# Kernel tuning notes

Measured on AMD Instinct MI355X. Metric: run time of the kernel, lower is better.

Reference implementation:

```python
import jax, jax.numpy as jnp
import numpy as np

HID = 256
BN_EPS = 1e-5
LN_EPS = 1e-5


def setup_inputs() -> dict:
    key = jax.random.key(0)
    ks = jax.random.split(key, 32)
    N, E, B = 50000, 400000, 2048
    F_ATOM, F_PROT = 70, 480

    def lin(k, fi, fo):
        return jax.random.normal(k, (fi, fo), jnp.float32) / np.sqrt(fi).astype(np.float32)

    inp = {
        "x": jax.random.normal(ks[0], (N, F_ATOM), jnp.float32),
        "edge_index": jax.random.randint(ks[1], (2, E), 0, N, jnp.int64),
        "batch": jnp.sort(jax.random.randint(ks[2], (N,), 0, B, jnp.int64)),
        "protein_emb": jax.random.normal(ks[3], (B, F_PROT), jnp.float32),
        # GIN layer 0 (70 -> 256)
        "gin0_w1": lin(ks[4], F_ATOM, HID), "gin0_b1": jnp.zeros((HID,), jnp.float32),
        "gin0_w2": lin(ks[5], HID, HID),    "gin0_b2": jnp.zeros((HID,), jnp.float32),
        "gin0_gamma": jnp.ones((HID,), jnp.float32), "gin0_beta": jnp.zeros((HID,), jnp.float32),
        # GIN layers 1..3 stacked (256 -> 256)
        "gin_w1": jnp.stack([lin(ks[6 + i], HID, HID) for i in range(3)]),
        "gin_b1": jnp.zeros((3, HID), jnp.float32),
        "gin_w2": jnp.stack([lin(ks[9 + i], HID, HID) for i in range(3)]),
        "gin_b2": jnp.zeros((3, HID), jnp.float32),
        "gin_gamma": jnp.ones((3, HID), jnp.float32),
        "gin_beta": jnp.zeros((3, HID), jnp.float32),
        # protein projector
        "wp": lin(ks[12], F_PROT, HID), "bp": jnp.zeros((HID,), jnp.float32),
        "ln_g": jnp.ones((HID,), jnp.float32), "ln_b": jnp.zeros((HID,), jnp.float32),
        # predictor MLP
        "wpr1": lin(ks[13], 2 * HID, 1024), "bpr1": jnp.zeros((1024,), jnp.float32),
        "wpr2": lin(ks[14], 1024, 512),     "bpr2": jnp.zeros((512,), jnp.float32),
        "wpr3": lin(ks[15], 512, 1),        "bpr3": jnp.zeros((1,), jnp.float32),
    }
    return inp


def _gin_layer(h, src, dst, n_nodes, w1, b1, w2, b2, gamma, beta):
    # GINConv (eps=0): mlp(x + sum_{j->i} x_j); scatter-add over destination
    agg = jax.ops.segment_sum(h[src], dst, num_segments=n_nodes)
    z = h + agg
    z = jax.nn.relu(z @ w1 + b1) @ w2 + b2
    # BatchNorm1d in eval mode: running_mean=0, running_var=1
    z = z * (gamma / np.sqrt(1.0 + BN_EPS).astype(np.float32)) + beta
    return jax.nn.relu(z)  # dropout is identity in eval


def reference(x, edge_index, batch, protein_emb,
              gin0_w1, gin0_b1, gin0_w2, gin0_b2, gin0_gamma, gin0_beta,
              gin_w1, gin_b1, gin_w2, gin_b2, gin_gamma, gin_beta,
              wp, bp, ln_g, ln_b,
              wpr1, bpr1, wpr2, bpr2, wpr3, bpr3):
    n_nodes = x.shape[0]
    n_graphs = protein_emb.shape[0]
    src, dst = edge_index[0], edge_index[1]

    h = _gin_layer(x, src, dst, n_nodes, gin0_w1, gin0_b1, gin0_w2, gin0_b2, gin0_gamma, gin0_beta)
    for i in range(3):  # layers 1..3 with residual
        h = h + _gin_layer(h, src, dst, n_nodes,
                           gin_w1[i], gin_b1[i], gin_w2[i], gin_b2[i], gin_gamma[i], gin_beta[i])

    # global_add_pool over graph ids
    drug_vec = jax.ops.segment_sum(h, batch, num_segments=n_graphs)  # [B, 256]

    # protein projector: Linear -> LayerNorm -> ReLU (dropout identity)
    p = protein_emb @ wp + bp
    mu = jnp.mean(p, axis=-1, keepdims=True)
    var = jnp.var(p, axis=-1, keepdims=True)
    p = (p - mu) * jax.lax.rsqrt(var + LN_EPS) * ln_g + ln_b
    prot_vec = jax.nn.relu(p)

    cat = jnp.concatenate([drug_vec, prot_vec], axis=1)  # [B, 512]
    h1 = jax.nn.relu(cat @ wpr1 + bpr1)
    h2 = jax.nn.relu(h1 @ wpr2 + bpr2)
    return h2 @ wpr3 + bpr3  # [B, 1]
```

## Files before the change

### kernel.cpp

```cpp
#include <hip/hip_runtime.h>

#define F_ATOM 70

#define FLAG_RELU 1
#define FLAG_BN   2
#define FLAG_RES  4

typedef __attribute__((ext_vector_type(8))) short short8;
typedef __attribute__((ext_vector_type(4))) float floatx4;

__device__ __forceinline__ float bf2f(unsigned short u) {
    union { unsigned int i; float f; } x; x.i = (unsigned int)u << 16; return x.f;
}
__device__ __forceinline__ unsigned short f2bf(float f) {
    union { float f; unsigned int i; } x; x.f = f;
    unsigned int r = x.i + 0x7fffu + ((x.i >> 16) & 1u);
    return (unsigned short)(r >> 16);
}
__device__ __forceinline__ float blo(unsigned int u){ union{unsigned int a; float f;}x; x.a=u<<16; return x.f; }
__device__ __forceinline__ float bhi(unsigned int u){ union{unsigned int a; float f;}x; x.a=u&0xffff0000u; return x.f; }


__global__ void count_kernel(const int* __restrict__ dst, int* __restrict__ cnt, int E) {
    int i = blockIdx.x * blockDim.x + threadIdx.x;
    if (i < E) atomicAdd(&cnt[dst[i]], 1);
}

__global__ void scan_kernel(const int* __restrict__ cnt, int* __restrict__ offs, int n) {
    __shared__ int wsum[16];
    __shared__ int carry_s;
    int t = threadIdx.x, lane = t & 63, wid = t >> 6;
    if (t == 0) carry_s = 0;
    __syncthreads();
    for (int base = 0; base < n; base += 1024) {
        int idx = base + t;
        int v = (idx < n) ? cnt[idx] : 0;
        int s = v;
        #pragma unroll
        for (int o = 1; o < 64; o <<= 1) {
            int x = __shfl_up(s, o);
            if (lane >= o) s += x;
        }
        if (lane == 63) wsum[wid] = s;
        __syncthreads();
        int woff = 0;
        #pragma unroll
        for (int wI = 0; wI < 16; ++wI) woff += (wI < wid) ? wsum[wI] : 0;
        int carry = carry_s;
        if (idx < n) offs[idx] = carry + woff + s - v;
        __syncthreads();
        if (t == 1023) carry_s = carry + woff + s;
        __syncthreads();
    }
    if (threadIdx.x == 0) offs[n] = carry_s;
}

__global__ void fill_kernel(const int* __restrict__ src, const int* __restrict__ dst,
                            const int* __restrict__ offs, int* __restrict__ cursor,
                            int* __restrict__ ssrc, int E) {
    int i = blockIdx.x * blockDim.x + threadIdx.x;
    if (i < E) {
        int d = dst[i];
        int pos = atomicAdd(&cursor[d], 1);
        ssrc[offs[d] + pos] = src[i];
    }
}

__global__ void graph_bounds_kernel(const int* __restrict__ batch, int* __restrict__ goffs,
                                    int N, int B) {
    int g = blockIdx.x * blockDim.x + threadIdx.x;
    if (g > B) return;
    int lo = 0, hi = N;
    while (lo < hi) {
        int mid = (lo + hi) >> 1;
        if (batch[mid] < g) lo = mid + 1; else hi = mid;
    }
    goffs[g] = lo;
}


__global__ __launch_bounds__(256) void prep_kernel(
    const float* __restrict__ x, const float* __restrict__ pemb,
    const float* __restrict__ g0w1, const float* __restrict__ g0w2,
    const float* __restrict__ gw1, const float* __restrict__ gw2,
    const float* __restrict__ wp, const float* __restrict__ wpr1, const float* __restrict__ wpr2,
    unsigned short* __restrict__ xb, unsigned short* __restrict__ pembbf,
    unsigned short* __restrict__ w10t, unsigned short* __restrict__ w20t,
    unsigned short* __restrict__ w1t, unsigned short* __restrict__ w2t,
    unsigned short* __restrict__ wpt, unsigned short* __restrict__ wpr1t,
    unsigned short* __restrict__ wpr2t, int N, int B)
{
    const long long sz0 = (long long)N * 80;
    const long long sz1 = (long long)B * 480;
    const long long szw10 = 256 * 128, szw20 = 256 * 256;
    const long long szw1 = 3 * 256 * 256, szw2 = 3 * 256 * 256;
    const long long szwp = 256 * 480, szp1 = 1024 * 512, szp2 = 512 * 1024;
    const long long total = sz0 + sz1 + szw10 + szw20 + szw1 + szw2 + szwp + szp1 + szp2;
    const long long stride = (long long)gridDim.x * blockDim.x;
    for (long long idx = (long long)blockIdx.x * blockDim.x + threadIdx.x; idx < total; idx += stride) {
        long long r = idx;
        if (r < sz0) {
            int node = (int)(r / 80), f = (int)(r - (long long)node * 80);
            xb[r] = f2bf(f < F_ATOM ? x[(long long)node * F_ATOM + f] : 0.f);
            continue;
        }
        r -= sz0;
        if (r < sz1) { pembbf[r] = f2bf(pemb[r]); continue; }
        r -= sz1;
        if (r < szw10) {
            int nr = (int)(r >> 7), k = (int)(r & 127);
            w10t[r] = f2bf(k < F_ATOM ? g0w1[k * 256 + nr] : 0.f);
            continue;
        }
        r -= szw10;
        if (r < szw20) {
            int nr = (int)(r >> 8), k = (int)(r & 255);
            w20t[r] = f2bf(g0w2[k * 256 + nr]);
            continue;
        }
        r -= szw20;
        if (r < szw1) {
            int l = (int)(r >> 16); int r2 = (int)(r & 65535);
            int nr = r2 >> 8, k = r2 & 255;
            w1t[r] = f2bf(gw1[(size_t)l * 65536 + k * 256 + nr]);
            continue;
        }
        r -= szw1;
        if (r < szw2) {
            int l = (int)(r >> 16); int r2 = (int)(r & 65535);
            int nr = r2 >> 8, k = r2 & 255;
            w2t[r] = f2bf(gw2[(size_t)l * 65536 + k * 256 + nr]);
            continue;
        }
        r -= szw2;
        if (r < szwp) {
            int nr = (int)(r / 480), k = (int)(r - (long long)nr * 480);
            wpt[r] = f2bf(wp[k * 256 + nr]);
            continue;
        }
        r -= szwp;
        if (r < szp1) {
            int nr = (int)(r >> 9), k = (int)(r & 511);
            wpr1t[r] = f2bf(wpr1[k * 1024 + nr]);
            continue;
        }
        r -= szp1;
        {
            int nr = (int)(r >> 10), k = (int)(r & 1023);
            wpr2t[r] = f2bf(wpr2[k * 512 + nr]);
        }
    }
}

__global__ __launch_bounds__(256) void agg0b_kernel(
    const unsigned short* __restrict__ xb, const int* __restrict__ offs,
    const int* __restrict__ ssrc, unsigned short* __restrict__ z0, int n) {
    int t = threadIdx.x;
    int node = blockIdx.x * 16 + (t >> 4);
    if (node >= n) return;
    int c = t & 15;
    if (c >= 10) {
        *(uint4*)(z0 + (size_t)node * 128 + c * 8) = make_uint4(0, 0, 0, 0);
        return;
    }
    const unsigned short* base = xb + (size_t)node * 80 + c * 8;
    uint4 v = *(const uint4*)base;
    float a[8];
    a[0]=blo(v.x); a[1]=bhi(v.x); a[2]=blo(v.y); a[3]=bhi(v.y);
    a[4]=blo(v.z); a[5]=bhi(v.z); a[6]=blo(v.w); a[7]=bhi(v.w);
    int s = offs[node], e2 = offs[node + 1];
    int k = s;
    for (; k + 3 < e2; k += 4) {
        uint4 u0 = *(const uint4*)(xb + (size_t)ssrc[k]     * 80 + c * 8);
        uint4 u1 = *(const uint4*)(xb + (size_t)ssrc[k + 1] * 80 + c * 8);
        uint4 u2 = *(const uint4*)(xb + (size_t)ssrc[k + 2] * 80 + c * 8);
        uint4 u3 = *(const uint4*)(xb + (size_t)ssrc[k + 3] * 80 + c * 8);
        a[0]+=blo(u0.x); a[1]+=bhi(u0.x); a[2]+=blo(u0.y); a[3]+=bhi(u0.y);
        a[4]+=blo(u0.z); a[5]+=bhi(u0.z); a[6]+=blo(u0.w); a[7]+=bhi(u0.w);
        a[0]+=blo(u1.x); a[1]+=bhi(u1.x); a[2]+=blo(u1.y); a[3]+=bhi(u1.y);
        a[4]+=blo(u1.z); a[5]+=bhi(u1.z); a[6]+=blo(u1.w); a[7]+=bhi(u1.w);
        a[0]+=blo(u2.x); a[1]+=bhi(u2.x); a[2]+=blo(u2.y); a[3]+=bhi(u2.y);
        a[4]+=blo(u2.z); a[5]+=bhi(u2.z); a[6]+=blo(u2.w); a[7]+=bhi(u2.w);
        a[0]+=blo(u3.x); a[1]+=bhi(u3.x); a[2]+=blo(u3.y); a[3]+=bhi(u3.y);
        a[4]+=blo(u3.z); a[5]+=bhi(u3.z); a[6]+=blo(u3.w); a[7]+=bhi(u3.w);
    }
    for (; k < e2; ++k) {
        uint4 u0 = *(const uint4*)(xb + (size_t)ssrc[k] * 80 + c * 8);
        a[0]+=blo(u0.x); a[1]+=bhi(u0.x); a[2]+=blo(u0.y); a[3]+=bhi(u0.y);
        a[4]+=blo(u0.z); a[5]+=bhi(u0.z); a[6]+=blo(u0.w); a[7]+=bhi(u0.w);
    }
    unsigned int o0 = (unsigned int)f2bf(a[0]) | ((unsigned int)f2bf(a[1]) << 16);
    unsigned int o1 = (unsigned int)f2bf(a[2]) | ((unsigned int)f2bf(a[3]) << 16);
    unsigned int o2 = (unsigned int)f2bf(a[4]) | ((unsigned int)f2bf(a[5]) << 16);
    unsigned int o3 = (unsigned int)f2bf(a[6]) | ((unsigned int)f2bf(a[7]) << 16);
    *(uint4*)(z0 + (size_t)node * 128 + c * 8) = make_uint4(o0, o1, o2, o3);
}

__global__ __launch_bounds__(256) void agg_bf16_kernel(
    const unsigned short* __restrict__ h, const int* __restrict__ offs,
    const int* __restrict__ ssrc, unsigned short* __restrict__ out, int n) {
    int t = threadIdx.x;
    int node = blockIdx.x * 8 + (t >> 5);
    if (node >= n) return;
    int f8 = (t & 31) * 8;
    uint4 v = *(const uint4*)(h + (size_t)node * 256 + f8);
    float a[8];
    a[0]=blo(v.x); a[1]=bhi(v.x); a[2]=blo(v.y); a[3]=bhi(v.y);
    a[4]=blo(v.z); a[5]=bhi(v.z); a[6]=blo(v.w); a[7]=bhi(v.w);
    int s = offs[node], e2 = offs[node + 1];
    int k = s;
    for (; k + 3 < e2; k += 4) {
        uint4 u0 = *(const uint4*)(h + (size_t)ssrc[k]     * 256 + f8);
        uint4 u1 = *(const uint4*)(h + (size_t)ssrc[k + 1] * 256 + f8);
        uint4 u2 = *(const uint4*)(h + (size_t)ssrc[k + 2] * 256 + f8);
        uint4 u3 = *(const uint4*)(h + (size_t)ssrc[k + 3] * 256 + f8);
        a[0]+=blo(u0.x); a[1]+=bhi(u0.x); a[2]+=blo(u0.y); a[3]+=bhi(u0.y);
        a[4]+=blo(u0.z); a[5]+=bhi(u0.z); a[6]+=blo(u0.w); a[7]+=bhi(u0.w);
        a[0]+=blo(u1.x); a[1]+=bhi(u1.x); a[2]+=blo(u1.y); a[3]+=bhi(u1.y);
        a[4]+=blo(u1.z); a[5]+=bhi(u1.z); a[6]+=blo(u1.w); a[7]+=bhi(u1.w);
        a[0]+=blo(u2.x); a[1]+=bhi(u2.x); a[2]+=blo(u2.y); a[3]+=bhi(u2.y);
        a[4]+=blo(u2.z); a[5]+=bhi(u2.z); a[6]+=blo(u2.w); a[7]+=bhi(u2.w);
        a[0]+=blo(u3.x); a[1]+=bhi(u3.x); a[2]+=blo(u3.y); a[3]+=bhi(u3.y);
        a[4]+=blo(u3.z); a[5]+=bhi(u3.z); a[6]+=blo(u3.w); a[7]+=bhi(u3.w);
    }
    for (; k < e2; ++k) {
        uint4 u0 = *(const uint4*)(h + (size_t)ssrc[k] * 256 + f8);
        a[0]+=blo(u0.x); a[1]+=bhi(u0.x); a[2]+=blo(u0.y); a[3]+=bhi(u0.y);
        a[4]+=blo(u0.z); a[5]+=bhi(u0.z); a[6]+=blo(u0.w); a[7]+=bhi(u0.w);
    }
    unsigned int o0 = (unsigned int)f2bf(a[0]) | ((unsigned int)f2bf(a[1]) << 16);
    unsigned int o1 = (unsigned int)f2bf(a[2]) | ((unsigned int)f2bf(a[3]) << 16);
    unsigned int o2 = (unsigned int)f2bf(a[4]) | ((unsigned int)f2bf(a[5]) << 16);
    unsigned int o3 = (unsigned int)f2bf(a[6]) | ((unsigned int)f2bf(a[7]) << 16);
    *(uint4*)(out + (size_t)node * 256 + f8) = make_uint4(o0, o1, o2, o3);
}


template<int KSH>
__global__ __launch_bounds__(256, 4) void fused_gin(
    const unsigned short* __restrict__ Z, const unsigned short* __restrict__ W1,
    const float* __restrict__ b1, const unsigned short* __restrict__ W2,
    const float* __restrict__ b2, const float* __restrict__ bng,
    const float* __restrict__ bnb, const unsigned short* __restrict__ res,
    unsigned short* __restrict__ out, int M)
{
    constexpr int CPR = KSH / 8;
    constexpr int NT1 = KSH / 32;
    __shared__ unsigned short sZ[64 * 256];
    const int T = threadIdx.x;
    const int lane = T & 63;
    const int wc = T >> 6;
    const int fr = lane & 15, hi = lane >> 4;
    const int crow = hi * 4;
    const int row0 = blockIdx.x * 64;

    #pragma unroll
    for (int i = 0; i < (64 * CPR) / 256; ++i) {
        int c = T + i * 256;
        int row = c / CPR, p = c % CPR;
        int pp = p ^ (row & 15);
        int gr = row0 + row; if (gr > M - 1) gr = M - 1;
        __builtin_amdgcn_global_load_lds(
            (const __attribute__((address_space(1))) void*)(Z + (size_t)gr * KSH + pp * 8),
            (__attribute__((address_space(3))) void*)&sZ[c * 8], 16, 0, 0);
    }
    __syncthreads();

    floatx4 acc[4][4];
    #pragma unroll
    for (int m = 0; m < 4; ++m)
        #pragma unroll
        for (int n = 0; n < 4; ++n)
            acc[m][n] = (floatx4){0.f, 0.f, 0.f, 0.f};

    {
        short8 cur[4], nxt[4];
        #pragma unroll
        for (int n = 0; n < 4; ++n)
            cur[n] = *(const short8*)(W1 + (size_t)(wc * 64 + n * 16 + fr) * KSH + hi * 8);
        #pragma unroll
        for (int kk = 0; kk < NT1; ++kk) {
            if (kk + 1 < NT1) {
                #pragma unroll
                for (int n = 0; n < 4; ++n)
                    nxt[n] = *(const short8*)(W1 + (size_t)(wc * 64 + n * 16 + fr) * KSH + (kk + 1) * 32 + hi * 8);
            }
            short8 af[4];
            #pragma unroll
            for (int m = 0; m < 4; ++m) {
                int r = m * 16 + fr;
                int byte = r * (KSH * 2) + ((kk * 64 + hi * 16) ^ ((r & 15) << 4));
                af[m] = *(const short8*)((const char*)sZ + byte);
            }
            #pragma unroll
            for (int m = 0; m < 4; ++m)
                #pragma unroll
                for (int n = 0; n < 4; ++n)
                    acc[m][n] = __builtin_amdgcn_mfma_f32_16x16x32_bf16(af[m], cur[n], acc[m][n], 0, 0, 0);
            #pragma unroll
            for (int n = 0; n < 4; ++n) cur[n] = nxt[n];
        }
    }
    __syncthreads();

    #pragma unroll
    for (int n = 0; n < 4; ++n) {
        int col = wc * 64 + n * 16 + fr;
        float bb = b1[col];
        #pragma unroll
        for (int m = 0; m < 4; ++m) {
            #pragma unroll
            for (int j = 0; j < 4; ++j) {
                int r = m * 16 + crow + j;
                float y = fmaxf(acc[m][n][j] + bb, 0.f);
                int byte = r * 512 + ((col * 2) ^ ((r & 15) << 4));
                *(unsigned short*)((char*)sZ + byte) = f2bf(y);
            }
        }
    }
    __syncthreads();

    #pragma unroll
    for (int m = 0; m < 4; ++m)
        #pragma unroll
        for (int n = 0; n < 4; ++n)
            acc[m][n] = (floatx4){0.f, 0.f, 0.f, 0.f};
    {
        short8 cur[4], nxt[4];
        #pragma unroll
        for (int n = 0; n < 4; ++n)
            cur[n] = *(const short8*)(W2 + (size_t)(wc * 64 + n * 16 + fr) * 256 + hi * 8);
        #pragma unroll
        for (int kk = 0; kk < 8; ++kk) {
            if (kk < 7) {
                #pragma unroll
                for (int n = 0; n < 4; ++n)
                    nxt[n] = *(const short8*)(W2 + (size_t)(wc * 64 + n * 16 + fr) * 256 + (kk + 1) * 32 + hi * 8);
            }
            short8 af[4];
            #pragma unroll
            for (int m = 0; m < 4; ++m) {
                int r = m * 16 + fr;
                int byte = r * 512 + ((kk * 64 + hi * 16) ^ ((r & 15) << 4));
                af[m] = *(const short8*)((const char*)sZ + byte);
            }
            #pragma unroll
            for (int m = 0; m < 4; ++m)
                #pragma unroll
                for (int n = 0; n < 4; ++n)
                    acc[m][n] = __builtin_amdgcn_mfma_f32_16x16x32_bf16(af[m], cur[n], acc[m][n], 0, 0, 0);
            #pragma unroll
            for (int n = 0; n < 4; ++n) cur[n] = nxt[n];
        }
    }
    __syncthreads();

    {
        const float inv = rsqrtf(1.f + 1e-5f);
        #pragma unroll
        for (int n = 0; n < 4; ++n) {
            int col = wc * 64 + n * 16 + fr;
            float bb = b2[col];
            float sc = bng[col] * inv, be = bnb[col];
            #pragma unroll
            for (int m = 0; m < 4; ++m) {
                #pragma unroll
                for (int j = 0; j < 4; ++j) {
                    int r = m * 16 + crow + j;
                    float y = (acc[m][n][j] + bb) * sc + be;
                    y = fmaxf(y, 0.f);
                    int byte = r * 512 + ((col * 2) ^ ((r & 15) << 4));
                    *(unsigned short*)((char*)sZ + byte) = f2bf(y);
                }
            }
        }
    }
    __syncthreads();

    #pragma unroll
    for (int i = 0; i < 8; ++i) {
        int c = T + i * 256;
        int row = c >> 5, slot = c & 31;
        int gr = row0 + row;
        if (gr >= M) continue;
        int byte = row * 512 + ((slot * 16) ^ ((row & 15) << 4));
        short8 v = *(const short8*)((const char*)sZ + byte);
        if (res) {
            short8 rv = *(const short8*)(res + (size_t)gr * 256 + slot * 8);
            #pragma unroll
            for (int e = 0; e < 8; ++e) {
                float f = bf2f((unsigned short)v[e]) + bf2f((unsigned short)rv[e]);
                v[e] = (short)f2bf(f);
            }
        }
        *(short8*)(out + (size_t)gr * 256 + slot * 8) = v;
    }
}


__global__ __launch_bounds__(256) void mfma_gemm(
    const unsigned short* __restrict__ A, const unsigned short* __restrict__ Bt,
    const float* __restrict__ bias, const float* __restrict__ bng,
    const float* __restrict__ bnb, const unsigned short* __restrict__ res,
    unsigned short* __restrict__ out, int M, int K, int NC, int flags)
{
    __shared__ unsigned short sA[2][128 * 32];
    __shared__ unsigned short sB[2][128 * 32];
    const int T = threadIdx.x;
    const int lane = T & 63;
    const int w = T >> 6, wr = w >> 1, wc = w & 1;
    const int row0 = blockIdx.x * 128;
    const int col0 = blockIdx.y * 128;
    const int nt = K >> 5;

    floatx4 acc[4][4];
    #pragma unroll
    for (int m = 0; m < 4; ++m)
        #pragma unroll
        for (int n = 0; n < 4; ++n)
            acc[m][n] = (floatx4){0.f, 0.f, 0.f, 0.f};

    auto stage = [&](int buf, int k0) {
        #pragma unroll
        for (int it = 0; it < 2; ++it) {
            int c = T + it * 256;
            int r = c >> 2, p = c & 3;
            int gr = row0 + r; if (gr > M - 1) gr = M - 1;
            const unsigned short* gA = A + (size_t)gr * K + k0 + p * 8;
            __builtin_amdgcn_global_load_lds(
                (const __attribute__((address_space(1))) void*)gA,
                (__attribute__((address_space(3))) void*)&sA[buf][c * 8], 16, 0, 0);
            const unsigned short* gB = Bt + (size_t)(col0 + r) * K + k0 + p * 8;
            __builtin_amdgcn_global_load_lds(
                (const __attribute__((address_space(1))) void*)gB,
                (__attribute__((address_space(3))) void*)&sB[buf][c * 8], 16, 0, 0);
        }
    };

    auto compute = [&](int buf) {
        const int fr = lane & 15;
        const int kh = (lane >> 4) * 8;
        short8 af[4], bv[4];
        #pragma unroll
        for (int m = 0; m < 4; ++m)
            af[m] = *(const short8*)&sA[buf][(wr * 64 + m * 16 + fr) * 32 + kh];
        #pragma unroll
        for (int n = 0; n < 4; ++n)
            bv[n] = *(const short8*)&sB[buf][(wc * 64 + n * 16 + fr) * 32 + kh];
        #pragma unroll
        for (int m = 0; m < 4; ++m)
            #pragma unroll
            for (int n = 0; n < 4; ++n)
                acc[m][n] = __builtin_amdgcn_mfma_f32_16x16x32_bf16(af[m], bv[n], acc[m][n], 0, 0, 0);
    };

    stage(0, 0);
    __syncthreads();
    int cur = 0;
    for (int t = 0; t < nt - 1; ++t) {
        stage(cur ^ 1, (t + 1) * 32);
        compute(cur);
        __syncthreads();
        cur ^= 1;
    }
    compute(cur);

    const int crow = (lane >> 4) * 4;
    const int ccol = lane & 15;
    const float inv = rsqrtf(1.f + 1e-5f);
    #pragma unroll
    for (int n = 0; n < 4; ++n) {
        int col = col0 + wc * 64 + n * 16 + ccol;
        float bb = bias ? bias[col] : 0.f;
        float sc = 1.f, be = 0.f;
        if (flags & FLAG_BN) { sc = bng[col] * inv; be = bnb[col]; }
        #pragma unroll
        for (int m = 0; m < 4; ++m) {
            #pragma unroll
            for (int j = 0; j < 4; ++j) {
                int r = row0 + wr * 64 + m * 16 + crow + j;
                if (r >= M) continue;
                float y = acc[m][n][j] + bb;
                if (flags & FLAG_BN) y = y * sc + be;
                if (flags & FLAG_RELU) y = fmaxf(y, 0.f);
                if (flags & FLAG_RES) y += bf2f(res[(size_t)r * NC + col]);
                out[(size_t)r * NC + col] = f2bf(y);
            }
        }
    }
}


__global__ void pool_kernel(const unsigned short* __restrict__ h, const int* __restrict__ goffs,
                            unsigned short* __restrict__ out, int ldout) {
    int g = blockIdx.x;
    int f = threadIdx.x;
    int s = goffs[g], e = goffs[g + 1];
    float acc = 0.f;
    for (int i = s; i < e; ++i) acc += bf2f(h[(size_t)i * 256 + f]);
    out[(size_t)g * ldout + f] = f2bf(acc);
}

__global__ void ln_relu_kernel(const unsigned short* __restrict__ p, const float* __restrict__ g,
                               const float* __restrict__ b, unsigned short* __restrict__ out, int ldout) {
    int row = blockIdx.x;
    int t = threadIdx.x;
    float v = bf2f(p[(size_t)row * 256 + t]);
    float s1 = v, s2 = v * v;
    #pragma unroll
    for (int o = 32; o > 0; o >>= 1) { s1 += __shfl_xor(s1, o); s2 += __shfl_xor(s2, o); }
    __shared__ float as1[4], as2[4];
    int w = t >> 6, lane = t & 63;
    if (lane == 0) { as1[w] = s1; as2[w] = s2; }
    __syncthreads();
    float tot1 = as1[0] + as1[1] + as1[2] + as1[3];
    float tot2 = as2[0] + as2[1] + as2[2] + as2[3];
    float mean = tot1 * (1.f / 256.f);
    float var = tot2 * (1.f / 256.f) - mean * mean;
    float y = (v - mean) * rsqrtf(var + 1e-5f) * g[t] + b[t];
    out[(size_t)row * ldout + t] = f2bf(fmaxf(y, 0.f));
}

__global__ void pred3_kernel(const unsigned short* __restrict__ h2, const float* __restrict__ w,
                             const float* __restrict__ b, float* __restrict__ out, int B) {
    int row = blockIdx.x * 4 + (threadIdx.x >> 6);
    int lane = threadIdx.x & 63;
    if (row >= B) return;
    float acc = 0.f;
    #pragma unroll
    for (int k = 0; k < 512; k += 64) acc += bf2f(h2[(size_t)row * 512 + k + lane]) * w[k + lane];
    #pragma unroll
    for (int o = 32; o > 0; o >>= 1) acc += __shfl_xor(acc, o);
    if (lane == 0) out[row] = acc + b[0];
}


extern "C" void kernel_launch(void* const* d_in, const int* in_sizes, int n_in,
                              void* d_out, int out_size, void* d_ws, size_t ws_size,
                              hipStream_t stream) {
    const float* x    = (const float*)d_in[0];
    const int*   ei   = (const int*)d_in[1];
    const int*   batch= (const int*)d_in[2];
    const float* pemb = (const float*)d_in[3];
    const float* g0w1 = (const float*)d_in[4];
    const float* g0b1 = (const float*)d_in[5];
    const float* g0w2 = (const float*)d_in[6];
    const float* g0b2 = (const float*)d_in[7];
    const float* g0g  = (const float*)d_in[8];
    const float* g0be = (const float*)d_in[9];
    const float* gw1  = (const float*)d_in[10];
    const float* gb1  = (const float*)d_in[11];
    const float* gw2  = (const float*)d_in[12];
    const float* gb2  = (const float*)d_in[13];
    const float* gg   = (const float*)d_in[14];
    const float* gbe  = (const float*)d_in[15];
    const float* wp   = (const float*)d_in[16];
    const float* bp   = (const float*)d_in[17];
    const float* lng  = (const float*)d_in[18];
    const float* lnb  = (const float*)d_in[19];
    const float* wpr1 = (const float*)d_in[20];
    const float* bpr1 = (const float*)d_in[21];
    const float* wpr2 = (const float*)d_in[22];
    const float* bpr2 = (const float*)d_in[23];
    const float* wpr3 = (const float*)d_in[24];
    const float* bpr3 = (const float*)d_in[25];

    int N = in_sizes[0] / F_ATOM;
    int E = in_sizes[1] / 2;
    int B = in_sizes[3] / 480;

    char* wsp = (char*)d_ws;
    auto carve = [&](size_t bytes) {
        void* p = (void*)wsp;
        wsp += (bytes + 255) & ~(size_t)255;
        return p;
    };
    int* offs   = (int*)carve((size_t)(N + 1) * 4);
    int* cursor = (int*)carve((size_t)N * 4);
    int* ssrc   = (int*)carve((size_t)E * 4);
    int* goffs  = (int*)carve((size_t)(B + 1) * 4);
    unsigned short* xb   = (unsigned short*)carve((size_t)N * 80 * 2);
    unsigned short* z0   = (unsigned short*)carve((size_t)N * 128 * 2);
    unsigned short* hbuf = (unsigned short*)carve((size_t)N * 256 * 2);
    unsigned short* tbuf = (unsigned short*)carve((size_t)N * 256 * 2);
    unsigned short* zbuf = (unsigned short*)carve((size_t)N * 256 * 2);
    unsigned short* pembbf = (unsigned short*)carve((size_t)B * 480 * 2);
    unsigned short* ptmp = (unsigned short*)carve((size_t)B * 256 * 2);
    unsigned short* cat  = (unsigned short*)carve((size_t)B * 512 * 2);
    unsigned short* h1   = (unsigned short*)carve((size_t)B * 1024 * 2);
    unsigned short* h2   = (unsigned short*)carve((size_t)B * 512 * 2);
    unsigned short* w10t = (unsigned short*)carve((size_t)256 * 128 * 2);
    unsigned short* w20t = (unsigned short*)carve((size_t)256 * 256 * 2);
    unsigned short* w1t  = (unsigned short*)carve((size_t)3 * 256 * 256 * 2);
    unsigned short* w2t  = (unsigned short*)carve((size_t)3 * 256 * 256 * 2);
    unsigned short* wpt  = (unsigned short*)carve((size_t)256 * 480 * 2);
    unsigned short* wpr1t= (unsigned short*)carve((size_t)1024 * 512 * 2);
    unsigned short* wpr2t= (unsigned short*)carve((size_t)512 * 1024 * 2);

    const int* srcp = ei;
    const int* dstp = ei + E;

    hipMemsetAsync(cursor, 0, (size_t)N * 4, stream);
    count_kernel<<<(E + 255) / 256, 256, 0, stream>>>(dstp, cursor, E);
    scan_kernel<<<1, 1024, 0, stream>>>(cursor, offs, N);
    hipMemsetAsync(cursor, 0, (size_t)N * 4, stream);
    fill_kernel<<<(E + 255) / 256, 256, 0, stream>>>(srcp, dstp, offs, cursor, ssrc, E);
    graph_bounds_kernel<<<(B + 256) / 256, 256, 0, stream>>>(batch, goffs, N, B);

    prep_kernel<<<2048, 256, 0, stream>>>(x, pemb, g0w1, g0w2, gw1, gw2, wp, wpr1, wpr2,
                                          xb, pembbf, w10t, w20t, w1t, w2t, wpt, wpr1t, wpr2t,
                                          N, B);

    int rbN = (N + 63) / 64;

    agg0b_kernel<<<(N + 15) / 16, 256, 0, stream>>>(xb, offs, ssrc, z0, N);
    fused_gin<128><<<rbN, 256, 0, stream>>>(z0, w10t, g0b1, w20t, g0b2, g0g, g0be,
                                            nullptr, hbuf, N);

    unsigned short* H = hbuf; unsigned short* T2 = tbuf;
    for (int i = 0; i < 3; ++i) {
        agg_bf16_kernel<<<(N + 7) / 8, 256, 0, stream>>>(H, offs, ssrc, zbuf, N);
        fused_gin<256><<<rbN, 256, 0, stream>>>(zbuf, w1t + (size_t)i * 65536, gb1 + i * 256,
                                                w2t + (size_t)i * 65536, gb2 + i * 256,
                                                gg + i * 256, gbe + i * 256, H, T2, N);
        unsigned short* tmp = H; H = T2; T2 = tmp;
    }

    pool_kernel<<<B, 256, 0, stream>>>(H, goffs, cat, 512);

    mfma_gemm<<<dim3((B + 127) / 128, 2), 256, 0, stream>>>(pembbf, wpt, bp, nullptr, nullptr, nullptr,
                                                            ptmp, B, 480, 256, 0);
    ln_relu_kernel<<<B, 256, 0, stream>>>(ptmp, lng, lnb, cat + 256, 512);

    mfma_gemm<<<dim3((B + 127) / 128, 8), 256, 0, stream>>>(cat, wpr1t, bpr1, nullptr, nullptr, nullptr,
                                                            h1, B, 512, 1024, FLAG_RELU);
    mfma_gemm<<<dim3((B + 127) / 128, 4), 256, 0, stream>>>(h1, wpr2t, bpr2, nullptr, nullptr, nullptr,
                                                            h2, B, 1024, 512, FLAG_RELU);
    pred3_kernel<<<(B + 3) / 4, 256, 0, stream>>>(h2, wpr3, bpr3, (float*)d_out, B);
}
```

Measured before the change: 557.2 us.

## Parallelize CSR scan, reuse counts via atomicSub, deepen gather unroll, prefetch residual

Result: slower. 575.3 us (+3.3%).

```diff
diff --git a/kernel.cpp b/kernel.cpp
--- a/kernel.cpp
+++ b/kernel.cpp
@@ -26,33 +26,58 @@
     if (i < E) atomicAdd(&cnt[dst[i]], 1);
 }
 
-__global__ void scan_kernel(const int* __restrict__ cnt, int* __restrict__ offs, int n) {
+__global__ void scan_sum_kernel(const int* __restrict__ cnt, int* __restrict__ partial, int n) {
+    int t = threadIdx.x;
+    int base = blockIdx.x * 1024 + t * 4;
+    int v = 0;
+    #pragma unroll
+    for (int i = 0; i < 4; ++i) if (base + i < n) v += cnt[base + i];
+    #pragma unroll
+    for (int o = 32; o > 0; o >>= 1) v += __shfl_down(v, o);
+    __shared__ int ws[4];
+    if ((t & 63) == 0) ws[t >> 6] = v;
+    __syncthreads();
+    if (t == 0) partial[blockIdx.x] = ws[0] + ws[1] + ws[2] + ws[3];
+}
+
+__global__ void scan_part_kernel(int* __restrict__ partial, int nb) {
+    int t = threadIdx.x, lane = t & 63, w = t >> 6;
+    int v = (t < nb) ? partial[t] : 0;
+    int s = v;
+    #pragma unroll
+    for (int o = 1; o < 64; o <<= 1) { int x = __shfl_up(s, o); if (lane >= o) s += x; }
     __shared__ int wsum[16];
-    __shared__ int carry_s;
-    int t = threadIdx.x, lane = t & 63, wid = t >> 6;
-    if (t == 0) carry_s = 0;
-    __syncthreads();
-    for (int base = 0; base < n; base += 1024) {
-        int idx = base + t;
-        int v = (idx < n) ? cnt[idx] : 0;
-        int s = v;
-        #pragma unroll
-        for (int o = 1; o < 64; o <<= 1) {
-            int x = __shfl_up(s, o);
-            if (lane >= o) s += x;
-        }
-        if (lane == 63) wsum[wid] = s;
-        __syncthreads();
-        int woff = 0;
-        #pragma unroll
-        for (int wI = 0; wI < 16; ++wI) woff += (wI < wid) ? wsum[wI] : 0;
-        int carry = carry_s;
-        if (idx < n) offs[idx] = carry + woff + s - v;
-        __syncthreads();
-        if (t == 1023) carry_s = carry + woff + s;
-        __syncthreads();
-    }
-    if (threadIdx.x == 0) offs[n] = carry_s;
+    if (lane == 63) wsum[w] = s;
+    __syncthreads();
+    int woff = 0;
+    #pragma unroll
+    for (int i = 0; i < 16; ++i) woff += (i < w) ? wsum[i] : 0;
+    if (t < nb) partial[t] = woff + s - v;
+    if (t == 1023) partial[nb] = woff + s;
+}
+
+__global__ void scan_apply_kernel(const int* __restrict__ cnt, const int* __restrict__ partial,
+                                  int* __restrict__ offs, int n, int nb) {
+    int t = threadIdx.x;
+    int base = blockIdx.x * 1024 + t * 4;
+    int v[4];
+    #pragma unroll
+    for (int i = 0; i < 4; ++i) v[i] = (base + i < n) ? cnt[base + i] : 0;
+    int tsum = v[0] + v[1] + v[2] + v[3];
+    int lane = t & 63, w = t >> 6;
+    int s = tsum;
+    #pragma unroll
+    for (int o = 1; o < 64; o <<= 1) { int x = __shfl_up(s, o); if (lane >= o) s += x; }
+    __shared__ int wsum[4];
+    if (lane == 63) wsum[w] = s;
+    __syncthreads();
+    int woff = 0;
+    #pragma unroll
+    for (int i = 0; i < 4; ++i) woff += (i < w) ? wsum[i] : 0;
+    int run = partial[blockIdx.x] + woff + s - tsum;
+    #pragma unroll
+    for (int i = 0; i < 4; ++i) { if (base + i < n) offs[base + i] = run; run += v[i]; }
+    if (blockIdx.x == 0 && t == 0) offs[n] = partial[nb];
 }
 
 __global__ void fill_kernel(const int* __restrict__ src, const int* __restrict__ dst,
@@ -61,8 +86,8 @@
     int i = blockIdx.x * blockDim.x + threadIdx.x;
     if (i < E) {
         int d = dst[i];
-        int pos = atomicAdd(&cursor[d], 1);
-        ssrc[offs[d] + pos] = src[i];
+        int pos = atomicSub(&cursor[d], 1);
+        ssrc[offs[d] + pos - 1] = src[i];
     }
 }
 
@@ -152,6 +177,7 @@
     }
 }
 
+
 __global__ __launch_bounds__(256) void agg0b_kernel(
     const unsigned short* __restrict__ xb, const int* __restrict__ offs,
     const int* __restrict__ ssrc, unsigned short* __restrict__ z0, int n) {
@@ -163,28 +189,34 @@
         *(uint4*)(z0 + (size_t)node * 128 + c * 8) = make_uint4(0, 0, 0, 0);
         return;
     }
-    const unsigned short* base = xb + (size_t)node * 80 + c * 8;
-    uint4 v = *(const uint4*)base;
     float a[8];
-    a[0]=blo(v.x); a[1]=bhi(v.x); a[2]=blo(v.y); a[3]=bhi(v.y);
-    a[4]=blo(v.z); a[5]=bhi(v.z); a[6]=blo(v.w); a[7]=bhi(v.w);
+    {
+        uint4 v = *(const uint4*)(xb + (size_t)node * 80 + c * 8);
+        a[0]=blo(v.x); a[1]=bhi(v.x); a[2]=blo(v.y); a[3]=bhi(v.y);
+        a[4]=blo(v.z); a[5]=bhi(v.z); a[6]=blo(v.w); a[7]=bhi(v.w);
+    }
     int s = offs[node], e2 = offs[node + 1];
     int k = s;
-    for (; k + 3 < e2; k += 4) {
+    for (; k + 7 < e2; k += 8) {
+        uint4 u[8];
+        #pragma unroll
+        for (int q = 0; q < 8; ++q)
+            u[q] = *(const uint4*)(xb + (size_t)ssrc[k + q] * 80 + c * 8);
+        #pragma unroll
+        for (int q = 0; q < 8; ++q) {
+            a[0]+=blo(u[q].x); a[1]+=bhi(u[q].x); a[2]+=blo(u[q].y); a[3]+=bhi(u[q].y);
+            a[4]+=blo(u[q].z); a[5]+=bhi(u[q].z); a[6]+=blo(u[q].w); a[7]+=bhi(u[q].w);
+        }
+    }
+    for (; k + 1 < e2; k += 2) {
         uint4 u0 = *(const uint4*)(xb + (size_t)ssrc[k]     * 80 + c * 8);
         uint4 u1 = *(const uint4*)(xb + (size_t)ssrc[k + 1] * 80 + c * 8);
-        uint4 u2 = *(const uint4*)(xb + (size_t)ssrc[k + 2] * 80 + c * 8);
-        uint4 u3 = *(const uint4*)(xb + (size_t)ssrc[k + 3] * 80 + c * 8);
         a[0]+=blo(u0.x); a[1]+=bhi(u0.x); a[2]+=blo(u0.y); a[3]+=bhi(u0.y);
         a[4]+=blo(u0.z); a[5]+=bhi(u0.z); a[6]+=blo(u0.w); a[7]+=bhi(u0.w);
         a[0]+=blo(u1.x); a[1]+=bhi(u1.x); a[2]+=blo(u1.y); a[3]+=bhi(u1.y);
         a[4]+=blo(u1.z); a[5]+=bhi(u1.z); a[6]+=blo(u1.w); a[7]+=bhi(u1.w);
-        a[0]+=blo(u2.x); a[1]+=bhi(u2.x); a[2]+=blo(u2.y); a[3]+=bhi(u2.y);
-        a[4]+=blo(u2.z); a[5]+=bhi(u2.z); a[6]+=blo(u2.w); a[7]+=bhi(u2.w);
-        a[0]+=blo(u3.x); a[1]+=bhi(u3.x); a[2]+=blo(u3.y); a[3]+=bhi(u3.y);
-        a[4]+=blo(u3.z); a[5]+=bhi(u3.z); a[6]+=blo(u3.w); a[7]+=bhi(u3.w);
-    }
-    for (; k < e2; ++k) {
+    }
+    if (k < e2) {
         uint4 u0 = *(const uint4*)(xb + (size_t)ssrc[k] * 80 + c * 8);
         a[0]+=blo(u0.x); a[1]+=bhi(u0.x); a[2]+=blo(u0.y); a[3]+=bhi(u0.y);
         a[4]+=blo(u0.z); a[5]+=bhi(u0.z); a[6]+=blo(u0.w); a[7]+=bhi(u0.w);
@@ -203,27 +235,34 @@
     int node = blockIdx.x * 8 + (t >> 5);
     if (node >= n) return;
     int f8 = (t & 31) * 8;
-    uint4 v = *(const uint4*)(h + (size_t)node * 256 + f8);
     float a[8];
-    a[0]=blo(v.x); a[1]=bhi(v.x); a[2]=blo(v.y); a[3]=bhi(v.y);
-    a[4]=blo(v.z); a[5]=bhi(v.z); a[6]=blo(v.w); a[7]=bhi(v.w);
+    {
+        uint4 v = *(const uint4*)(h + (size_t)node * 256 + f8);
+        a[0]=blo(v.x); a[1]=bhi(v.x); a[2]=blo(v.y); a[3]=bhi(v.y);
+        a[4]=blo(v.z); a[5]=bhi(v.z); a[6]=blo(v.w); a[7]=bhi(v.w);
+    }
     int s = offs[node], e2 = offs[node + 1];
     int k = s;
-    for (; k + 3 < e2; k += 4) {
+    for (; k + 7 < e2; k += 8) {
+        uint4 u[8];
+        #pragma unroll
+        for (int q = 0; q < 8; ++q)
+            u[q] = *(const uint4*)(h + (size_t)ssrc[k + q] * 256 + f8);
+        #pragma unroll
+        for (int q = 0; q < 8; ++q) {
+            a[0]+=blo(u[q].x); a[1]+=bhi(u[q].x); a[2]+=blo(u[q].y); a[3]+=bhi(u[q].y);
+            a[4]+=blo(u[q].z); a[5]+=bhi(u[q].z); a[6]+=blo(u[q].w); a[7]+=bhi(u[q].w);
+        }
+    }
+    for (; k + 1 < e2; k += 2) {
         uint4 u0 = *(const uint4*)(h + (size_t)ssrc[k]     * 256 + f8);
         uint4 u1 = *(const uint4*)(h + (size_t)ssrc[k + 1] * 256 + f8);
-        uint4 u2 = *(const uint4*)(h + (size_t)ssrc[k + 2] * 256 + f8);
-        uint4 u3 = *(const uint4*)(h + (size_t)ssrc[k + 3] * 256 + f8);
         a[0]+=blo(u0.x); a[1]+=bhi(u0.x); a[2]+=blo(u0.y); a[3]+=bhi(u0.y);
         a[4]+=blo(u0.z); a[5]+=bhi(u0.z); a[6]+=blo(u0.w); a[7]+=bhi(u0.w);
         a[0]+=blo(u1.x); a[1]+=bhi(u1.x); a[2]+=blo(u1.y); a[3]+=bhi(u1.y);
         a[4]+=blo(u1.z); a[5]+=bhi(u1.z); a[6]+=blo(u1.w); a[7]+=bhi(u1.w);
-        a[0]+=blo(u2.x); a[1]+=bhi(u2.x); a[2]+=blo(u2.y); a[3]+=bhi(u2.y);
-        a[4]+=blo(u2.z); a[5]+=bhi(u2.z); a[6]+=blo(u2.w); a[7]+=bhi(u2.w);
-        a[0]+=blo(u3.x); a[1]+=bhi(u3.x); a[2]+=blo(u3.y); a[3]+=bhi(u3.y);
-        a[4]+=blo(u3.z); a[5]+=bhi(u3.z); a[6]+=blo(u3.w); a[7]+=bhi(u3.w);
-    }
-    for (; k < e2; ++k) {
+    }
+    if (k < e2) {
         uint4 u0 = *(const uint4*)(h + (size_t)ssrc[k] * 256 + f8);
         a[0]+=blo(u0.x); a[1]+=bhi(u0.x); a[2]+=blo(u0.y); a[3]+=bhi(u0.y);
         a[4]+=blo(u0.z); a[5]+=bhi(u0.z); a[6]+=blo(u0.w); a[7]+=bhi(u0.w);
@@ -254,6 +293,17 @@
     const int crow = hi * 4;
     const int row0 = blockIdx.x * 64;
 
+    short8 resv[8];
+    if (res) {
+        #pragma unroll
+        for (int i = 0; i < 8; ++i) {
+            int c = T + i * 256;
+            int row = c >> 5, slot = c & 31;
+            int gr = row0 + row; if (gr > M - 1) gr = M - 1;
+            resv[i] = *(const short8*)(res + (size_t)gr * 256 + slot * 8);
+        }
+    }
+
     #pragma unroll
     for (int i = 0; i < (64 * CPR) / 256; ++i) {
         int c = T + i * 256;
@@ -386,10 +436,9 @@
         int byte = row * 512 + ((slot * 16) ^ ((row & 15) << 4));
         short8 v = *(const short8*)((const char*)sZ + byte);
         if (res) {
-            short8 rv = *(const short8*)(res + (size_t)gr * 256 + slot * 8);
             #pragma unroll
             for (int e = 0; e < 8; ++e) {
-                float f = bf2f((unsigned short)v[e]) + bf2f((unsigned short)rv[e]);
+                float f = bf2f((unsigned short)v[e]) + bf2f((unsigned short)resv[i][e]);
                 v[e] = (short)f2bf(f);
             }
         }
@@ -575,10 +624,11 @@
         wsp += (bytes + 255) & ~(size_t)255;
         return p;
     };
-    int* offs   = (int*)carve((size_t)(N + 1) * 4);
-    int* cursor = (int*)carve((size_t)N * 4);
-    int* ssrc   = (int*)carve((size_t)E * 4);
-    int* goffs  = (int*)carve((size_t)(B + 1) * 4);
+    int* offs    = (int*)carve((size_t)(N + 1) * 4);
+    int* cursor  = (int*)carve((size_t)N * 4);
+    int* partial = (int*)carve((size_t)1025 * 4);
+    int* ssrc    = (int*)carve((size_t)E * 4);
+    int* goffs   = (int*)carve((size_t)(B + 1) * 4);
     unsigned short* xb   = (unsigned short*)carve((size_t)N * 80 * 2);
     unsigned short* z0   = (unsigned short*)carve((size_t)N * 128 * 2);
     unsigned short* hbuf = (unsigned short*)carve((size_t)N * 256 * 2);
@@ -602,8 +652,10 @@
 
     hipMemsetAsync(cursor, 0, (size_t)N * 4, stream);
     count_kernel<<<(E + 255) / 256, 256, 0, stream>>>(dstp, cursor, E);
-    scan_kernel<<<1, 1024, 0, stream>>>(cursor, offs, N);
-    hipMemsetAsync(cursor, 0, (size_t)N * 4, stream);
+    int nb = (N + 1023) / 1024;
+    scan_sum_kernel<<<nb, 256, 0, stream>>>(cursor, partial, N);
+    scan_part_kernel<<<1, 1024, 0, stream>>>(partial, nb);
+    scan_apply_kernel<<<nb, 256, 0, stream>>>(cursor, partial, offs, N, nb);
     fill_kernel<<<(E + 255) / 256, 256, 0, stream>>>(srcp, dstp, offs, cursor, ssrc, E);
     graph_bounds_kernel<<<(B + 256) / 256, 256, 0, stream>>>(batch, goffs, N, B);
 
```
